# Optimization experiments

Measured on AMD Instinct MI355X. Metric: run time of the kernel, lower is better.

## Reference

```python
import jax, jax.numpy as jnp
import numpy as np

# Fixed model constants from setParams()
TAU_W, TAU_N, TAU_R = 1.5e6, 6.0e5, 6.0e4
TAU_E, TAU_G, TAU_A = 2.5e4, 1.0e4, 1.0e4
F_W_MAX, F_N_MAX, F_R_MAX = 6.5, 5.0, 5.0
ALPHA_W, ALPHA_N, ALPHA_R = 0.5, 0.175, 0.13
BETA_W, BETA_R = -0.4, -0.9
GAMMA_E, GAMMA_G, GAMMA_A = 5.0, 4.0, 2.0
H_MAX, THETA_W = 1.0, 2.0
TAU_HW, TAU_HS = 3.483e7, 3.06e7
KAPPA = 1.5
A_RK = (0.5, 0.5, 1.0, 1.0)

T, B = 10000, 512


def setup_inputs() -> dict:
    key = jax.random.key(0)
    noise = 0.05 * jax.random.normal(key, (T, B), dtype=jnp.float32)
    return {
        "noise_input": noise,
        "g_RRe": jnp.float32(1.3),
        "g_RWe": jnp.float32(1.6),
        "g_WNi": jnp.float32(-2.0),
        "g_WRi": jnp.float32(-4.0),
        "g_NRi": jnp.float32(-1.3),
        "g_NWi": jnp.float32(-1.68),
    }


def _heaviside(x):
    # smooth heaviside: sigmoid with steepness 5
    return jax.nn.sigmoid(5.0 * x)


def reference(noise_input, g_RRe, g_RWe, g_WNi, g_WRi, g_NRi, g_NWi):
    b = noise_input.shape[1]
    dt = noise_input.dtype
    init = (
        jnp.full((b,), 6.0, dt),    # f_W
        jnp.full((b,), 1e-3, dt),   # f_N
        jnp.full((b,), 1e-3, dt),   # f_R
        jnp.full((b,), 0.9, dt),    # c_WXi
        jnp.full((b,), 1e-3, dt),   # c_NXi
        jnp.full((b,), 1e-3, dt),   # c_RXe
        jnp.full((b,), 0.5, dt),    # h
    )

    def step(state, noise):
        fW0, fN0, fR0, cW0, cN0, cR0, h0 = state
        # RK moment lists; index 0 is the step's initial value
        fW = [fW0]; fN = [fN0]; fR = [fR0]
        cW = [cW0]; cN = [cN0]; cR = [cR0]; hh = [h0]
        for n in range(4):
            a = A_RK[n]
            I_W = g_NWi * cN[n] + g_RWe * cR[n] + noise
            I_N = g_WNi * cW[n] + noise
            I_R = g_WRi * cW[n] + g_NRi * cN[n] + g_RRe * cR[n] + noise
            fW.append(fW[0] + a * (F_W_MAX * 0.5 * (1.0 + jnp.tanh((I_W - BETA_W) / ALPHA_W)) - fW[n]) / TAU_W)
            fN.append(fN[0] + a * (F_N_MAX * 0.5 * (1.0 + jnp.tanh((I_N + KAPPA * hh[n]) / ALPHA_N)) - fN[n]) / TAU_N)
            fR.append(fR[0] + a * (F_R_MAX * 0.5 * (1.0 + jnp.tanh((I_R - BETA_R) / ALPHA_R)) - fR[n]) / TAU_R)
            cW.append(cW[0] + a * (jnp.tanh(fW[n + 1] / GAMMA_E) - cW[n]) / TAU_E)
            cN.append(cN[0] + a * (jnp.tanh(fN[n + 1] / GAMMA_G) - cN[n]) / TAU_G)
            cR.append(cR[0] + a * (jnp.tanh(fR[n + 1] / GAMMA_A) - cR[n]) / TAU_A)
            hh.append(hh[0] + a * ((H_MAX - hh[n]) / TAU_HW * _heaviside(fW[n] - THETA_W)
                                   - hh[n] / TAU_HS * _heaviside(THETA_W - fW[n])))
        comb = lambda v: (-3.0 * v[0] + 2.0 * v[1] + 4.0 * v[2] + 2.0 * v[3] + v[4]) / 6.0
        new_state = tuple(comb(v) for v in (fW, fN, fR, cW, cN, cR, hh))
        return new_state, jnp.stack(new_state)  # [7, B]

    _, traj = jax.lax.scan(step, init, noise_input)
    return traj  # [T, 7, B]
```

## Files before the change

kernel.cpp:

```cpp
#include <hip/hip_runtime.h>

#define T_STEPS 10000
#define BATCH   512

__device__ __forceinline__ float fexp2(float x) {
#if __has_builtin(__builtin_amdgcn_exp2f)
  return __builtin_amdgcn_exp2f(x);
#else
  return exp2f(x);
#endif
}

__device__ __forceinline__ float frcp(float x) {
#if __has_builtin(__builtin_amdgcn_rcpf)
  return __builtin_amdgcn_rcpf(x);
#else
  return 1.0f / x;
#endif
}

#define PIN(x) asm volatile("" : "+v"(x))

template <int CTRL>
__device__ __forceinline__ float qperm(float v) {
  int i = __builtin_bit_cast(int, v);
#if __has_builtin(__builtin_amdgcn_mov_dpp)
  int r = __builtin_amdgcn_mov_dpp(i, CTRL, 0xF, 0xF, true);
#else
  int r = __builtin_amdgcn_ds_swizzle(i, 0x8000 | CTRL);
#endif
  return __builtin_bit_cast(float, r);
}

__global__ __launch_bounds__(64, 1)
void sleep_rk4_kernel(const float* __restrict__ noise,
                      const float* __restrict__ pgRRe,
                      const float* __restrict__ pgRWe,
                      const float* __restrict__ pgWNi,
                      const float* __restrict__ pgWRi,
                      const float* __restrict__ pgNRi,
                      const float* __restrict__ pgNWi,
                      float* __restrict__ out)
{
  const int tid  = (int)(blockIdx.x * 64u + threadIdx.x);
  const int b    = tid >> 2;
  const int role = tid & 3;

  const float g_RRe = *pgRRe, g_RWe = *pgRWe, g_WNi = *pgWNi;
  const float g_WRi = *pgWRi, g_NRi = *pgNRi, g_NWi = *pgNWi;

  const float L2E = 1.4426950408889634f;
  const float LN2 = 0.6931471805599453f;

  float W1, W2, W3, NSC, BB, qa, qb, pa, pb, cs, ia, ib;
  float f0, c0;
  int v0i, v1i;
  bool dostore1, role03;

  if (role == 0) {
    const float SC = 2.0f * L2E / 0.5f;
    W1 = SC * g_NWi; W2 = SC * g_RWe; W3 = 0.0f; NSC = SC; BB = SC * 0.4f;
    qa = -1.0f / 1.5e6f; qb = 6.5f / 1.5e6f; pa = 0.0f; pb = -6.5f / 1.5e6f;
    cs = 2.0f * L2E / 5.0f; ia = -1.0f / 2.5e4f; ib = 1.0f / 2.5e4f;
    f0 = 6.0f; c0 = 0.9f; v0i = 0; v1i = 3; dostore1 = true;  role03 = true;
  } else if (role == 1) {
    const float SC = 2.0f * L2E / 0.175f;
    W1 = SC * g_WNi; W2 = SC * 1.5f; W3 = 0.0f; NSC = SC; BB = 0.0f;
    qa = -1.0f / 6.0e5f; qb = 5.0f / 6.0e5f; pa = 0.0f; pb = -5.0f / 6.0e5f;
    cs = 2.0f * L2E / 4.0f; ia = -1.0f / 1.0e4f; ib = 1.0f / 1.0e4f;
    f0 = 1.0e-3f; c0 = 1.0e-3f; v0i = 1; v1i = 4; dostore1 = true;  role03 = false;
  } else if (role == 2) {
    const float SC = 2.0f * L2E / 0.13f;
    W1 = SC * g_WRi; W2 = SC * g_NRi; W3 = SC * g_RRe; NSC = SC; BB = SC * 0.9f;
    qa = -1.0f / 6.0e4f; qb = 5.0f / 6.0e4f; pa = 0.0f; pb = -5.0f / 6.0e4f;
    cs = 2.0f * L2E / 2.0f; ia = -1.0f / 1.0e4f; ib = 1.0f / 1.0e4f;
    f0 = 1.0e-3f; c0 = 1.0e-3f; v0i = 2; v1i = 5; dostore1 = true;  role03 = false;
  } else {
    W1 = 0.0f; W2 = -5.0f * L2E; W3 = 0.0f; NSC = 0.0f; BB = 10.0f * L2E;
    qa = -1.0f / 3.06e7f; qb = 0.0f;
    pa = (1.0f / 3.06e7f - 1.0f / 3.483e7f);
    pb = 1.0f / 3.483e7f;
    cs = 0.0f; ia = 0.0f; ib = 0.0f;
    f0 = 0.5f; c0 = 0.0f; v0i = 6; v1i = 6; dostore1 = false; role03 = true;
  }

  const float AQAh = 0.5f * qa, AQA1 = qa;
  const float AIAh = 0.5f * ia, AIA1 = ia;
  const float IAC  = ia * cs;
  const float TIA  = 2.0f * ia;
  const float R6   = 0.16666666666666666f;

  float vF[4], vG[4];
  auto frun = [&](float f0b, float Gb, float* v) -> float {
    const float Chb = fmaf(0.5f, Gb, f0b), C1b = f0b + Gb;
    float s0 = f0b, acc = -3.0f * f0b;
    s0 = fmaf(AQAh, s0, Chb); v[0] = s0; acc = fmaf(2.0f, s0, acc);
    s0 = fmaf(AQAh, s0, Chb); v[1] = s0; acc = fmaf(4.0f, s0, acc);
    s0 = fmaf(AQA1, s0, C1b); v[2] = s0; acc = fmaf(2.0f, s0, acc);
    s0 = fmaf(AQA1, s0, C1b); v[3] = s0; acc = fmaf(1.0f, s0, acc);
    float q = acc * R6; q = fmaf(fmaf(q, -6.0f, acc), R6, q); return q;
  };
  const float KF = frun(1.0f, 0.0f, vF);
  const float KG = frun(0.0f, 1.0f, vG);

  auto crun = [&](const float* v, float c0b, float e1u, float vd1) -> float {
    const float E1h = IAC * e1u, E11 = 2.0f * IAC * e1u;
    const float Dh = c0b + 0.5f * vd1, D1 = c0b + vd1;
    float s1 = c0b, acc = -3.0f * c0b;
    s1 = fmaf(AIAh, s1, fmaf(E1h, v[0], Dh)); acc = fmaf(2.0f, s1, acc);
    s1 = fmaf(AIAh, s1, fmaf(E1h, v[1], Dh)); acc = fmaf(4.0f, s1, acc);
    s1 = fmaf(AIA1, s1, fmaf(E11, v[2], D1)); acc = fmaf(2.0f, s1, acc);
    s1 = fmaf(AIA1, s1, fmaf(E11, v[3], D1)); acc = fmaf(1.0f, s1, acc);
    float q = acc * R6; q = fmaf(fmaf(q, -6.0f, acc), R6, q); return q;
  };
  float z4[4] = {0.0f, 0.0f, 0.0f, 0.0f};
  const float KC  = crun(z4, 1.0f, 0.0f, 0.0f);
  const float LAf = crun(vF, 0.0f, 1.0f, 0.0f);
  const float LBf = crun(vG, 0.0f, 1.0f, 0.0f);
  const float KW  = crun(z4, 0.0f, 0.0f, 1.0f);

  float LAe, LBe, VDK, Pc, tLAe, tLBe, tVDK, tP;
  auto crefresh_compute = [&](float fcur) {
    const float zb = cs * fcur;
    const float ez = fexp2(zb);
    const float sc_ = frcp(1.0f + ez);
    const float t2 = fmaf(sc_, sc_, -sc_);
    const float e1 = LN2 * t2;
    const float vC = fmaf(-e1, zb, sc_);
    const float VD1 = fmaf(TIA, vC, ib);
    tLAe = LAf * e1; tLBe = LBf * e1; tVDK = KW * VD1;
    tP = fmaf(pa, fcur, pb);
  };
  crefresh_compute(f0);
  LAe = tLAe; LBe = tLBe; VDK = tVDK; Pc = tP;

  float dF = 0.0f, dC = 0.0f;
  float Gq0, Gq1, Gq2, Gq3;

  const int off0 = v0i * BATCH + b;
  const int off1 = v1i * BATCH + b;
  float* obase = out;

  float nb0[16], nb1[16];
#pragma unroll
  for (int j = 0; j < 16; ++j) nb0[j] = noise[b + j * BATCH];

  {
    const float pubS = role03 ? f0 : c0;
    const float xAs = qperm<0x01>(c0);
    const float xBs = qperm<0x1E>(pubS);
    const float YB = fmaf(W1, xAs, fmaf(W2, xBs, fmaf(W3, c0, BB)));
    Gq0 = fmaf(Pc, frcp(1.0f + fexp2(fmaf(NSC, nb0[0], YB))), qb);
    Gq1 = fmaf(Pc, frcp(1.0f + fexp2(fmaf(NSC, nb0[1], YB))), qb);
    Gq2 = fmaf(Pc, frcp(1.0f + fexp2(fmaf(NSC, nb0[2], YB))), qb);
    Gq3 = fmaf(Pc, frcp(1.0f + fexp2(fmaf(NSC, nb0[3], YB))), qb);
  }

  auto GROUP = [&](float n0, float n1, float n2, float n3) {
    const float t0 = KG * Gq0, t1 = KG * Gq1, t2 = KG * Gq2, t3 = KG * Gq3;
    const float pubS = role03 ? f0 : c0;
    const float pubD = role03 ? dF : dC;
    const float xAs = qperm<0x01>(c0);
    const float xBs = qperm<0x1E>(pubS);
    const float xAd = qperm<0x01>(dC);
    const float xBd = qperm<0x1E>(pubD);
    const float f1 = fmaf(KF, f0, t0);
    float YB = fmaf(W3, c0, BB);
    float dY = W3 * dC;
    const float c1 = fmaf(KC, c0, fmaf(LAe, f0, fmaf(LBe, Gq0, VDK)));
    YB = fmaf(W2, xBs, YB);
    dY = fmaf(W2, xBd, dY);
    const float f2 = fmaf(KF, f1, t1);
    YB = fmaf(W1, xAs, YB);
    dY = fmaf(W1, xAd, dY);
    const float c2 = fmaf(KC, c1, fmaf(LAe, f1, fmaf(LBe, Gq1, VDK)));
    const float y0 = fmaf(NSC, n0, fmaf(4.5f, dY, YB));
    const float y1 = fmaf(NSC, n1, fmaf(5.5f, dY, YB));
    const float f3 = fmaf(KF, f2, t2);
    const float y2 = fmaf(NSC, n2, fmaf(6.5f, dY, YB));
    const float y3 = fmaf(NSC, n3, fmaf(7.5f, dY, YB));
    const float c3 = fmaf(KC, c2, fmaf(LAe, f2, fmaf(LBe, Gq2, VDK)));
    const float e0 = fexp2(y0);
    const float e1_ = fexp2(y1);
    const float f4 = fmaf(KF, f3, t3);
    const float e2 = fexp2(y2);
    const float e3 = fexp2(y3);
    const float c4 = fmaf(KC, c3, fmaf(LAe, f3, fmaf(LBe, Gq3, VDK)));
    const float r0 = frcp(1.0f + e0);
    const float r1 = frcp(1.0f + e1_);
    const float r2 = frcp(1.0f + e2);
    const float r3 = frcp(1.0f + e3);
    obase[off0] = f1; obase[off1] = dostore1 ? c1 : f1; obase += 7 * BATCH;
    obase[off0] = f2; obase[off1] = dostore1 ? c2 : f2; obase += 7 * BATCH;
    obase[off0] = f3; obase[off1] = dostore1 ? c3 : f3; obase += 7 * BATCH;
    obase[off0] = f4; obase[off1] = dostore1 ? c4 : f4; obase += 7 * BATCH;
    Gq0 = fmaf(Pc, r0, qb);
    Gq1 = fmaf(Pc, r1, qb);
    Gq2 = fmaf(Pc, r2, qb);
    Gq3 = fmaf(Pc, r3, qb);
    dF = f4 - f3; dC = c4 - c3;
    f0 = f4; c0 = c4;
  };

  int base = 0;

#define TBLOCK(nbC, nbN)                                                      \
  do {                                                                        \
    int tl = base + 16; if (tl > T_STEPS - 16) tl = T_STEPS - 16;             \
    const float* __restrict__ lp = noise + (size_t)tl * BATCH;                \
    _Pragma("unroll")                                                         \
    for (int j = 0; j < 16; ++j) nbN[j] = lp[b + j * BATCH];                  \
    _Pragma("unroll")                                                         \
    for (int j = 0; j < 16; ++j) PIN(nbC[j]);                                 \
    crefresh_compute(f0);                                                     \
    GROUP(nbC[4], nbC[5], nbC[6], nbC[7]);                                    \
    LAe = tLAe; LBe = tLBe; VDK = tVDK; Pc = tP;                              \
    GROUP(nbC[8], nbC[9], nbC[10], nbC[11]);                                  \
    GROUP(nbC[12], nbC[13], nbC[14], nbC[15]);                                \
    PIN(nbN[0]); PIN(nbN[1]); PIN(nbN[2]); PIN(nbN[3]);                       \
    GROUP(nbN[0], nbN[1], nbN[2], nbN[3]);                                    \
    base += 16;                                                               \
  } while (0)

  for (int kk = 0; kk < 312; ++kk) {
    TBLOCK(nb0, nb1);
    TBLOCK(nb1, nb0);
  }
  TBLOCK(nb0, nb1);
#undef TBLOCK
}

extern "C" void kernel_launch(void* const* d_in, const int* in_sizes, int n_in,
                              void* d_out, int out_size, void* d_ws, size_t ws_size,
                              hipStream_t stream) {
  const float* noise = (const float*)d_in[0];
  const float* gRRe  = (const float*)d_in[1];
  const float* gRWe  = (const float*)d_in[2];
  const float* gWNi  = (const float*)d_in[3];
  const float* gWRi  = (const float*)d_in[4];
  const float* gNRi  = (const float*)d_in[5];
  const float* gNWi  = (const float*)d_in[6];
  float* out = (float*)d_out;

  sleep_rk4_kernel<<<dim3((BATCH * 4) / 64), dim3(64), 0, stream>>>(
      noise, gRRe, gRWe, gWNi, gWRi, gNRi, gNWi, out);
}
```

Measured before the change: 535.5 us.

## Stage outputs in LDS and flush as coalesced float4 stores; fold KG into constants

Each thread now writes its per-step results into a shared-memory tile covering 16 timesteps. At the end of every 16-step block the wave copies that tile to global memory with seven float4 stores per lane. Before, each step issued scattered scalar global stores, and the goal is fewer, wider, coalesced store instructions. Separately, the KG scaling is folded into the Pc/qb/LBf constants, which removes four multiplies per group. The risks are extra LDS traffic and possible LDS hazards: there is no barrier, since each wave owns its own slice of the tile.

```diff
diff --git a/kernel.cpp b/kernel.cpp
--- a/kernel.cpp
+++ b/kernel.cpp
@@ -42,8 +42,11 @@
                       const float* __restrict__ pgNWi,
                       float* __restrict__ out)
 {
+  __shared__ float shm[16 * 128];
+
   const int tid  = (int)(blockIdx.x * 64u + threadIdx.x);
   const int b    = tid >> 2;
+  const int bl   = b & 15;
   const int role = tid & 3;
 
   const float g_RRe = *pgRRe, g_RWe = *pgRWe, g_WNi = *pgWNi;
@@ -55,33 +58,33 @@
   float W1, W2, W3, NSC, BB, qa, qb, pa, pb, cs, ia, ib;
   float f0, c0;
   int v0i, v1i;
-  bool dostore1, role03;
+  bool role03;
 
   if (role == 0) {
     const float SC = 2.0f * L2E / 0.5f;
     W1 = SC * g_NWi; W2 = SC * g_RWe; W3 = 0.0f; NSC = SC; BB = SC * 0.4f;
     qa = -1.0f / 1.5e6f; qb = 6.5f / 1.5e6f; pa = 0.0f; pb = -6.5f / 1.5e6f;
     cs = 2.0f * L2E / 5.0f; ia = -1.0f / 2.5e4f; ib = 1.0f / 2.5e4f;
-    f0 = 6.0f; c0 = 0.9f; v0i = 0; v1i = 3; dostore1 = true;  role03 = true;
+    f0 = 6.0f; c0 = 0.9f; v0i = 0; v1i = 3; role03 = true;
   } else if (role == 1) {
     const float SC = 2.0f * L2E / 0.175f;
     W1 = SC * g_WNi; W2 = SC * 1.5f; W3 = 0.0f; NSC = SC; BB = 0.0f;
     qa = -1.0f / 6.0e5f; qb = 5.0f / 6.0e5f; pa = 0.0f; pb = -5.0f / 6.0e5f;
     cs = 2.0f * L2E / 4.0f; ia = -1.0f / 1.0e4f; ib = 1.0f / 1.0e4f;
-    f0 = 1.0e-3f; c0 = 1.0e-3f; v0i = 1; v1i = 4; dostore1 = true;  role03 = false;
+    f0 = 1.0e-3f; c0 = 1.0e-3f; v0i = 1; v1i = 4; role03 = false;
   } else if (role == 2) {
     const float SC = 2.0f * L2E / 0.13f;
     W1 = SC * g_WRi; W2 = SC * g_NRi; W3 = SC * g_RRe; NSC = SC; BB = SC * 0.9f;
     qa = -1.0f / 6.0e4f; qb = 5.0f / 6.0e4f; pa = 0.0f; pb = -5.0f / 6.0e4f;
     cs = 2.0f * L2E / 2.0f; ia = -1.0f / 1.0e4f; ib = 1.0f / 1.0e4f;
-    f0 = 1.0e-3f; c0 = 1.0e-3f; v0i = 2; v1i = 5; dostore1 = true;  role03 = false;
+    f0 = 1.0e-3f; c0 = 1.0e-3f; v0i = 2; v1i = 5; role03 = false;
   } else {
     W1 = 0.0f; W2 = -5.0f * L2E; W3 = 0.0f; NSC = 0.0f; BB = 10.0f * L2E;
     qa = -1.0f / 3.06e7f; qb = 0.0f;
     pa = (1.0f / 3.06e7f - 1.0f / 3.483e7f);
     pb = 1.0f / 3.483e7f;
     cs = 0.0f; ia = 0.0f; ib = 0.0f;
-    f0 = 0.5f; c0 = 0.0f; v0i = 6; v1i = 6; dostore1 = false; role03 = true;
+    f0 = 0.5f; c0 = 0.0f; v0i = 6; v1i = 7; role03 = true;
   }
 
   const float AQAh = 0.5f * qa, AQA1 = qa;
@@ -119,7 +122,11 @@
   const float LBf = crun(vG, 0.0f, 1.0f, 0.0f);
   const float KW  = crun(z4, 0.0f, 0.0f, 1.0f);
 
-  float LAe, LBe, VDK, Pc, tLAe, tLBe, tVDK, tP;
+  const float KGi  = 1.0f / KG;
+  const float LBfK = LBf * KGi;
+  const float qbK  = qb * KG;
+
+  float LAe, LBK, VDK, PK, tLAe, tLBK, tVDK, tPK;
   auto crefresh_compute = [&](float fcur) {
     const float zb = cs * fcur;
     const float ez = fexp2(zb);
@@ -128,18 +135,32 @@
     const float e1 = LN2 * t2;
     const float vC = fmaf(-e1, zb, sc_);
     const float VD1 = fmaf(TIA, vC, ib);
-    tLAe = LAf * e1; tLBe = LBf * e1; tVDK = KW * VD1;
-    tP = fmaf(pa, fcur, pb);
+    tLAe = LAf * e1; tLBK = LBfK * e1; tVDK = KW * VD1;
+    tPK = fmaf(pa, fcur, pb) * KG;
   };
   crefresh_compute(f0);
-  LAe = tLAe; LBe = tLBe; VDK = tVDK; Pc = tP;
+  LAe = tLAe; LBK = tLBK; VDK = tVDK; PK = tPK;
 
   float dF = 0.0f, dC = 0.0f;
   float Gq0, Gq1, Gq2, Gq3;
 
-  const int off0 = v0i * BATCH + b;
-  const int off1 = v1i * BATCH + b;
-  float* obase = out;
+  const int offA = v0i * 16 + bl;
+  const int offB = v1i * 16 + bl;
+
+  int ldoff[7], goff[7];
+  {
+    const int L = (int)threadIdx.x;
+    const int bb = (int)(blockIdx.x * 16u);
+#pragma unroll
+    for (int r = 0; r < 7; ++r) {
+      const int F  = r * 64 + L;
+      const int s_ = F / 28;
+      const int u  = F % 28;
+      ldoff[r] = s_ * 128 + u * 4;
+      goff[r]  = s_ * 3584 + (u >> 2) * 512 + (u & 3) * 4 + bb;
+    }
+  }
+  float* gflush = out;
 
   float nb0[16], nb1[16];
 #pragma unroll
@@ -150,54 +171,53 @@
     const float xAs = qperm<0x01>(c0);
     const float xBs = qperm<0x1E>(pubS);
     const float YB = fmaf(W1, xAs, fmaf(W2, xBs, fmaf(W3, c0, BB)));
-    Gq0 = fmaf(Pc, frcp(1.0f + fexp2(fmaf(NSC, nb0[0], YB))), qb);
-    Gq1 = fmaf(Pc, frcp(1.0f + fexp2(fmaf(NSC, nb0[1], YB))), qb);
-    Gq2 = fmaf(Pc, frcp(1.0f + fexp2(fmaf(NSC, nb0[2], YB))), qb);
-    Gq3 = fmaf(Pc, frcp(1.0f + fexp2(fmaf(NSC, nb0[3], YB))), qb);
-  }
-
-  auto GROUP = [&](float n0, float n1, float n2, float n3) {
-    const float t0 = KG * Gq0, t1 = KG * Gq1, t2 = KG * Gq2, t3 = KG * Gq3;
+    Gq0 = fmaf(PK, frcp(1.0f + fexp2(fmaf(NSC, nb0[0], YB))), qbK);
+    Gq1 = fmaf(PK, frcp(1.0f + fexp2(fmaf(NSC, nb0[1], YB))), qbK);
+    Gq2 = fmaf(PK, frcp(1.0f + fexp2(fmaf(NSC, nb0[2], YB))), qbK);
+    Gq3 = fmaf(PK, frcp(1.0f + fexp2(fmaf(NSC, nb0[3], YB))), qbK);
+  }
+
+  auto GROUP = [&](int SJ, float n0, float n1, float n2, float n3) {
     const float pubS = role03 ? f0 : c0;
     const float pubD = role03 ? dF : dC;
     const float xAs = qperm<0x01>(c0);
     const float xBs = qperm<0x1E>(pubS);
     const float xAd = qperm<0x01>(dC);
     const float xBd = qperm<0x1E>(pubD);
-    const float f1 = fmaf(KF, f0, t0);
+    const float f1 = fmaf(KF, f0, Gq0);
     float YB = fmaf(W3, c0, BB);
     float dY = W3 * dC;
-    const float c1 = fmaf(KC, c0, fmaf(LAe, f0, fmaf(LBe, Gq0, VDK)));
+    const float c1 = fmaf(KC, c0, fmaf(LAe, f0, fmaf(LBK, Gq0, VDK)));
     YB = fmaf(W2, xBs, YB);
     dY = fmaf(W2, xBd, dY);
-    const float f2 = fmaf(KF, f1, t1);
+    const float f2 = fmaf(KF, f1, Gq1);
     YB = fmaf(W1, xAs, YB);
     dY = fmaf(W1, xAd, dY);
-    const float c2 = fmaf(KC, c1, fmaf(LAe, f1, fmaf(LBe, Gq1, VDK)));
+    const float c2 = fmaf(KC, c1, fmaf(LAe, f1, fmaf(LBK, Gq1, VDK)));
     const float y0 = fmaf(NSC, n0, fmaf(4.5f, dY, YB));
     const float y1 = fmaf(NSC, n1, fmaf(5.5f, dY, YB));
-    const float f3 = fmaf(KF, f2, t2);
+    const float f3 = fmaf(KF, f2, Gq2);
     const float y2 = fmaf(NSC, n2, fmaf(6.5f, dY, YB));
     const float y3 = fmaf(NSC, n3, fmaf(7.5f, dY, YB));
-    const float c3 = fmaf(KC, c2, fmaf(LAe, f2, fmaf(LBe, Gq2, VDK)));
+    const float c3 = fmaf(KC, c2, fmaf(LAe, f2, fmaf(LBK, Gq2, VDK)));
     const float e0 = fexp2(y0);
     const float e1_ = fexp2(y1);
-    const float f4 = fmaf(KF, f3, t3);
+    const float f4 = fmaf(KF, f3, Gq3);
     const float e2 = fexp2(y2);
     const float e3 = fexp2(y3);
-    const float c4 = fmaf(KC, c3, fmaf(LAe, f3, fmaf(LBe, Gq3, VDK)));
+    const float c4 = fmaf(KC, c3, fmaf(LAe, f3, fmaf(LBK, Gq3, VDK)));
     const float r0 = frcp(1.0f + e0);
     const float r1 = frcp(1.0f + e1_);
     const float r2 = frcp(1.0f + e2);
     const float r3 = frcp(1.0f + e3);
-    obase[off0] = f1; obase[off1] = dostore1 ? c1 : f1; obase += 7 * BATCH;
-    obase[off0] = f2; obase[off1] = dostore1 ? c2 : f2; obase += 7 * BATCH;
-    obase[off0] = f3; obase[off1] = dostore1 ? c3 : f3; obase += 7 * BATCH;
-    obase[off0] = f4; obase[off1] = dostore1 ? c4 : f4; obase += 7 * BATCH;
-    Gq0 = fmaf(Pc, r0, qb);
-    Gq1 = fmaf(Pc, r1, qb);
-    Gq2 = fmaf(Pc, r2, qb);
-    Gq3 = fmaf(Pc, r3, qb);
+    shm[(SJ + 0) * 128 + offA] = f1;  shm[(SJ + 0) * 128 + offB] = c1;
+    shm[(SJ + 1) * 128 + offA] = f2;  shm[(SJ + 1) * 128 + offB] = c2;
+    shm[(SJ + 2) * 128 + offA] = f3;  shm[(SJ + 2) * 128 + offB] = c3;
+    shm[(SJ + 3) * 128 + offA] = f4;  shm[(SJ + 3) * 128 + offB] = c4;
+    Gq0 = fmaf(PK, r0, qbK);
+    Gq1 = fmaf(PK, r1, qbK);
+    Gq2 = fmaf(PK, r2, qbK);
+    Gq3 = fmaf(PK, r3, qbK);
     dF = f4 - f3; dC = c4 - c3;
     f0 = f4; c0 = c4;
   };
@@ -213,12 +233,18 @@
     _Pragma("unroll")                                                         \
     for (int j = 0; j < 16; ++j) PIN(nbC[j]);                                 \
     crefresh_compute(f0);                                                     \
-    GROUP(nbC[4], nbC[5], nbC[6], nbC[7]);                                    \
-    LAe = tLAe; LBe = tLBe; VDK = tVDK; Pc = tP;                              \
-    GROUP(nbC[8], nbC[9], nbC[10], nbC[11]);                                  \
-    GROUP(nbC[12], nbC[13], nbC[14], nbC[15]);                                \
+    GROUP(0, nbC[4], nbC[5], nbC[6], nbC[7]);                                 \
+    LAe = tLAe; LBK = tLBK; VDK = tVDK; PK = tPK;                             \
+    GROUP(4, nbC[8], nbC[9], nbC[10], nbC[11]);                               \
+    GROUP(8, nbC[12], nbC[13], nbC[14], nbC[15]);                             \
     PIN(nbN[0]); PIN(nbN[1]); PIN(nbN[2]); PIN(nbN[3]);                       \
-    GROUP(nbN[0], nbN[1], nbN[2], nbN[3]);                                    \
+    GROUP(12, nbN[0], nbN[1], nbN[2], nbN[3]);                                \
+    _Pragma("unroll")                                                         \
+    for (int r = 0; r < 7; ++r) {                                             \
+      const float4 vv = *(const float4*)&shm[ldoff[r]];                       \
+      *(float4*)&gflush[goff[r]] = vv;                                        \
+    }                                                                         \
+    gflush += 16 * 3584;                                                      \
     base += 16;                                                               \
   } while (0)
 
```

New measurement: 510.5 us. -4.7%, faster.
